# Performance work log

Measured on AMD Instinct MI355X. Metric: run time of the kernel, lower is better.

## Reference

```python
import jax, jax.numpy as jnp
import numpy as np

B, S, D, H, TM = 4, 512, 512, 8, 20
DH = D // H
LAMBDA_REG = 1e-3


def setup_inputs() -> dict:
    key = jax.random.key(0)
    ks = jax.random.split(key, 12)

    def lin(k, o, i):
        return (jax.random.normal(k, (o, i), jnp.float32) / np.float32(np.sqrt(i)))

    return {
        "x": jax.random.normal(ks[0], (B, S, D), jnp.float32),
        "Wq": lin(ks[1], D, D), "Wk": lin(ks[2], D, D), "Wv": lin(ks[3], D, D),
        "Wo": lin(ks[4], D, D), "bo": jnp.zeros((D,), jnp.float32),
        "gw1": lin(ks[5], 64, D), "gb1": jnp.zeros((64,), jnp.float32),
        "gw2": lin(ks[6], 32, 64), "gb2": jnp.zeros((32,), jnp.float32),
        "gw3": lin(ks[7], 1, 32), "gb3": jnp.zeros((1,), jnp.float32),
        "cw1": lin(ks[8], 32, D), "cb1": jnp.zeros((32,), jnp.float32),
        "cw2": lin(ks[9], 1, 32), "cb2": jnp.zeros((1,), jnp.float32),
        "alpha": jnp.float32(np.exp(-1.0 / 5.0)),   # tau_syn = 5
        "beta": jnp.float32(np.exp(-1.0 / 20.0)),   # tau_mem = 20
    }


def reference(x, Wq, Wk, Wv, Wo, bo, gw1, gb1, gw2, gb2, gw3, gb3,
              cw1, cb1, cw2, cb2, alpha, beta):
    scale = jnp.float32(DH ** -0.5)

    # adaptive window sizes T_i in [1, TM]
    g = jax.nn.sigmoid(jax.nn.relu(jax.nn.relu(x @ gw1.T + gb1) @ gw2.T + gb2) @ gw3.T + gb3)
    c = jax.nn.sigmoid(jax.nn.relu(x @ cw1.T + cb1) @ cw2.T + cb2)
    combined = (0.7 * g + 0.3 * c)[..., 0]                       # [B,S]
    T_i = jnp.clip(jnp.ceil(combined * TM), 1, TM).astype(jnp.int32)
    mask = (jnp.arange(TM)[None, None, :] < T_i[:, :, None]).astype(x.dtype)  # [B,S,TM]

    def lif_spikes(inp):  # inp [B,S,D] -> spikes [B,S,TM,D] (zeroed past T_i)
        def step(carry, _):
            v, i = carry
            i = alpha * i + inp
            v = beta * v + i
            s = jnp.where(v >= 1.0, 1.0, 0.0).astype(inp.dtype)
            v = v * (1.0 - s)  # v_reset = 0
            return (v, i), s
        z = jnp.zeros_like(inp)
        _, sp = jax.lax.scan(step, (z, z), None, length=TM)      # [TM,B,S,D]
        return jnp.moveaxis(sp, 0, 2) * mask[..., None]

    q_sp = lif_spikes(x @ Wq.T).reshape(B, S, TM, H, DH)
    k_sp = lif_spikes(x @ Wk.T).reshape(B, S, TM, H, DH)
    v_sp = lif_spikes(x @ Wv.T).reshape(B, S, TM, H, DH)

    scores = jnp.einsum('bithd,bjthd->bhij', q_sp, k_sp) * scale
    attn = jax.nn.softmax(scores, axis=-1)                       # dropout is eval-mode identity
    v_mean = v_sp.mean(axis=2).transpose(0, 2, 1, 3)             # [B,H,S,DH]
    out = jnp.einsum('bhij,bhjd->bhid', attn, v_mean)
    out = out.transpose(0, 2, 1, 3).reshape(B, S, D) @ Wo.T + bo
    reg = jnp.float32(LAMBDA_REG) * T_i.astype(x.dtype).mean()
    return out, attn, reg, T_i
```

## Files before the change

### kernel.cpp

```cpp
#include <hip/hip_runtime.h>
#include <cstdint>


typedef __attribute__((ext_vector_type(8))) _Float16 f16x8;
typedef __attribute__((ext_vector_type(4))) float f32x4;

__device__ __forceinline__ float sep_mad(float a, float b, float c) {
    float t = a * b;
    asm volatile("" : "+v"(t));
    return t + c;
}

union HU4 { _Float16 h[4]; ushort4 u; };
union HU8 { _Float16 h[8]; uint4 u; };

__device__ __forceinline__ void split4(float4 v, HU4& hi, HU4& lo) {
    hi.h[0] = (_Float16)v.x; lo.h[0] = (_Float16)(v.x - (float)hi.h[0]);
    hi.h[1] = (_Float16)v.y; lo.h[1] = (_Float16)(v.y - (float)hi.h[1]);
    hi.h[2] = (_Float16)v.z; lo.h[2] = (_Float16)(v.z - (float)hi.h[2]);
    hi.h[3] = (_Float16)v.w; lo.h[3] = (_Float16)(v.w - (float)hi.h[3]);
}

__global__ __launch_bounds__(256) void k_convert(
    const float* __restrict__ x,
    const float* __restrict__ Wq, const float* __restrict__ Wk,
    const float* __restrict__ Wv, const float* __restrict__ Wo,
    const float* __restrict__ gw1, const float* __restrict__ cw1,
    _Float16* __restrict__ xh, _Float16* __restrict__ xl,
    _Float16* __restrict__ WGh, _Float16* __restrict__ WGl,
    _Float16* __restrict__ Woh)
{
    const int t = blockIdx.x * 256 + threadIdx.x;
    HU4 hi, lo;
    if (t < 262144) {
        float4 v = ((const float4*)x)[t];
        split4(v, hi, lo);
        ((ushort4*)xh)[t] = hi.u;
        ((ushort4*)xl)[t] = lo.u;
        return;
    }
    const int t2 = t - 262144;
    if (t2 < 196608) {
        const int sel = t2 >> 16, o = t2 & 65535;
        const float* src = (sel == 0) ? Wq : ((sel == 1) ? Wk : Wv);
        float4 v = ((const float4*)src)[o];
        split4(v, hi, lo);
        ((ushort4*)WGh)[t2] = hi.u;
        ((ushort4*)WGl)[t2] = lo.u;
        return;
    }
    const int t3 = t2 - 196608;
    if (t3 < 12288) {
        const int row = t3 >> 7, c4 = t3 & 127;
        const float* src = (row < 64) ? (gw1 + row * 512) : (cw1 + (row - 64) * 512);
        float4 v = ((const float4*)src)[c4];
        split4(v, hi, lo);
        ((ushort4*)WGh)[196608 + t3] = hi.u;
        ((ushort4*)WGl)[196608 + t3] = lo.u;
        return;
    }
    const int t4 = t3 - 12288;
    if (t4 < 4096) {
        ushort4 z; z.x = z.y = z.z = z.w = 0;
        ((ushort4*)WGh)[208896 + t4] = z;
        ((ushort4*)WGl)[208896 + t4] = z;
        return;
    }
    const int t5 = t4 - 4096;
    float4 v = ((const float4*)Wo)[t5];
    split4(v, hi, lo);
    ((ushort4*)Woh)[t5] = hi.u;
}

__global__ __launch_bounds__(256) void k_gemm3(
    const _Float16* __restrict__ Ah, const _Float16* __restrict__ Al,
    const _Float16* __restrict__ Bh, const _Float16* __restrict__ Bl,
    float* __restrict__ Y)
{
    __shared__ _Float16 AsH[4][64][8];
    __shared__ _Float16 BsH[4][64][8];
    __shared__ _Float16 AsL[4][64][8];
    __shared__ _Float16 BsL[4][64][8];

    const int bn = blockIdx.x * 64, bm = blockIdx.y * 64;
    const int tid = threadIdx.x, w = tid >> 6, l = tid & 63;
    const int mB = (w & 1) * 32, nB = (w >> 1) * 32;
    const int sr = tid >> 2, sk = tid & 3;
    const int fr = l & 15, fk = l >> 4;

    f32x4 acc[2][2] = {};

    uint4 pAh = *(const uint4*)(Ah + (bm + sr) * 512 + sk * 8);
    uint4 pBh = *(const uint4*)(Bh + (bn + sr) * 512 + sk * 8);
    uint4 pAl = *(const uint4*)(Al + (bm + sr) * 512 + sk * 8);
    uint4 pBl = *(const uint4*)(Bl + (bn + sr) * 512 + sk * 8);

    for (int k0 = 0; k0 < 512; k0 += 32) {
        __syncthreads();
        *(uint4*)&AsH[sk][sr][0] = pAh;
        *(uint4*)&BsH[sk][sr][0] = pBh;
        *(uint4*)&AsL[sk][sr][0] = pAl;
        *(uint4*)&BsL[sk][sr][0] = pBl;
        __syncthreads();
        const int kn = (k0 + 32) & 511;
        pAh = *(const uint4*)(Ah + (bm + sr) * 512 + kn + sk * 8);
        pBh = *(const uint4*)(Bh + (bn + sr) * 512 + kn + sk * 8);
        pAl = *(const uint4*)(Al + (bm + sr) * 512 + kn + sk * 8);
        pBl = *(const uint4*)(Bl + (bn + sr) * 512 + kn + sk * 8);

        f16x8 ah[2], al[2];
#pragma unroll
        for (int mt = 0; mt < 2; mt++) {
            ah[mt] = *(const f16x8*)&AsH[fk][mB + mt * 16 + fr][0];
            al[mt] = *(const f16x8*)&AsL[fk][mB + mt * 16 + fr][0];
        }
#pragma unroll
        for (int nt = 0; nt < 2; nt++) {
            f16x8 bh = *(const f16x8*)&BsH[fk][nB + nt * 16 + fr][0];
            f16x8 bl = *(const f16x8*)&BsL[fk][nB + nt * 16 + fr][0];
#pragma unroll
            for (int mt = 0; mt < 2; mt++) {
                acc[mt][nt] = __builtin_amdgcn_mfma_f32_16x16x32_f16(ah[mt], bh, acc[mt][nt], 0, 0, 0);
                acc[mt][nt] = __builtin_amdgcn_mfma_f32_16x16x32_f16(ah[mt], bl, acc[mt][nt], 0, 0, 0);
                acc[mt][nt] = __builtin_amdgcn_mfma_f32_16x16x32_f16(al[mt], bh, acc[mt][nt], 0, 0, 0);
            }
        }
    }

#pragma unroll
    for (int mt = 0; mt < 2; mt++) {
#pragma unroll
        for (int nt = 0; nt < 2; nt++) {
            const int j = bn + nB + nt * 16 + fr;
#pragma unroll
            for (int rr = 0; rr < 4; rr++) {
                const int i = bm + mB + mt * 16 + fk * 4 + rr;
                Y[i * 1664 + j] = acc[mt][nt][rr];
            }
        }
    }
}

__global__ __launch_bounds__(256) void k_gates2(
    const float* __restrict__ h1raw,
    const float* __restrict__ gb1, const float* __restrict__ cb1,
    const float* __restrict__ gw2, const float* __restrict__ gb2,
    const float* __restrict__ gw3, const float* __restrict__ gb3,
    const float* __restrict__ cw2, const float* __restrict__ cb2,
    int* __restrict__ Ti, float* __restrict__ ti_out)
{
    __shared__ float h1s[32][100];
    __shared__ float w2s[32][65];
    __shared__ float h2s[32][36];
    const int tok0 = blockIdx.x * 32;
    const int tid = threadIdx.x;

    for (int i = tid; i < 2048; i += 256) w2s[i >> 6][i & 63] = gw2[i];
    for (int i = tid; i < 3072; i += 256) {
        const int r = i / 96, c = i % 96;
        const float v = h1raw[(long)(tok0 + r) * 1664 + c] + (c < 64 ? gb1[c] : cb1[c - 64]);
        h1s[r][c] = fmaxf(v, 0.f);
    }
    __syncthreads();

#pragma unroll
    for (int it = 0; it < 4; it++) {
        const int tok = (tid >> 5) + it * 8, o2 = tid & 31;
        float a = gb2[o2];
        for (int k = 0; k < 64; k++) a = fmaf(w2s[o2][k], h1s[tok][k], a);
        h2s[tok][o2] = fmaxf(a, 0.f);
    }
    __syncthreads();

    if (tid < 32) {
        const int tok = tid;
        float gg = gb3[0], cc = cb2[0];
        for (int k = 0; k < 32; k++) {
            gg = fmaf(gw3[k], h2s[tok][k], gg);
            cc = fmaf(cw2[k], h1s[tok][64 + k], cc);
        }
        float g = 1.f / (1.f + expf(-gg));
        float c = 1.f / (1.f + expf(-cc));
        float p1 = 0.7f * g, p2 = 0.3f * c;
        asm volatile("" : "+v"(p1), "+v"(p2));
        float comb = p1 + p2;
        float tf = ceilf(comb * 20.0f);
        tf = fminf(fmaxf(tf, 1.f), 20.f);
        Ti[tok0 + tok] = (int)tf;
        ti_out[tok0 + tok] = tf;
    }
}

template<int NCAT, bool BIAS>
__global__ __launch_bounds__(256) void k_gemm(
    const _Float16* __restrict__ A, const _Float16* __restrict__ B,
    const float* __restrict__ bias, float* __restrict__ Y)
{
    __shared__ _Float16 As[4][64][8];
    __shared__ _Float16 Bs[4][64][8];

    const int bn = blockIdx.x * 64, bm = blockIdx.y * 64;
    const int tid = threadIdx.x, w = tid >> 6, l = tid & 63;
    const int mB = (w & 1) * 32, nB = (w >> 1) * 32;
    const int sr = tid >> 2, sk = tid & 3;
    const int fr = l & 15, fk = l >> 4;

    f32x4 acc[2][2] = {};

    uint4 pA = *(const uint4*)(A + (bm + sr) * 512 + sk * 8);
    uint4 pB = *(const uint4*)(B + (bn + sr) * 512 + sk * 8);

    for (int k0 = 0; k0 < 512; k0 += 32) {
        __syncthreads();
        *(uint4*)&As[sk][sr][0] = pA;
        *(uint4*)&Bs[sk][sr][0] = pB;
        __syncthreads();
        const int kn = (k0 + 32) & 511;
        pA = *(const uint4*)(A + (bm + sr) * 512 + kn + sk * 8);
        pB = *(const uint4*)(B + (bn + sr) * 512 + kn + sk * 8);

        f16x8 ah[2];
#pragma unroll
        for (int mt = 0; mt < 2; mt++)
            ah[mt] = *(const f16x8*)&As[fk][mB + mt * 16 + fr][0];
#pragma unroll
        for (int nt = 0; nt < 2; nt++) {
            f16x8 bh = *(const f16x8*)&Bs[fk][nB + nt * 16 + fr][0];
#pragma unroll
            for (int mt = 0; mt < 2; mt++)
                acc[mt][nt] = __builtin_amdgcn_mfma_f32_16x16x32_f16(ah[mt], bh, acc[mt][nt], 0, 0, 0);
        }
    }

#pragma unroll
    for (int mt = 0; mt < 2; mt++) {
#pragma unroll
        for (int nt = 0; nt < 2; nt++) {
            const int j = bn + nB + nt * 16 + fr;
            float badd = BIAS ? bias[j] : 0.f;
#pragma unroll
            for (int rr = 0; rr < 4; rr++) {
                const int i = bm + mB + mt * 16 + fk * 4 + rr;
                Y[i * NCAT + j] = acc[mt][nt][rr] + badd;
            }
        }
    }
}

__global__ __launch_bounds__(256) void k_lif(
    const float* __restrict__ qkv,
    const int* __restrict__ Ti,
    const float* __restrict__ pAlpha, const float* __restrict__ pBeta,
    unsigned long long* __restrict__ qbits,
    unsigned long long* __restrict__ kbits,
    _Float16* __restrict__ vmT)
{
    __shared__ _Float16 cnts[64][18];
    const int wid = threadIdx.x >> 6, lane = threadIdx.x & 63;
    const int bh = blockIdx.y, s0 = blockIdx.x * 16;
    const int b = bh >> 3, h = bh & 7;
    const float alpha = pAlpha[0], beta = pBeta[0];

    const float* qrow0 = qkv + (long)(b * 512 + s0 + wid) * 1664 + h * 64 + lane;
    float cq = qrow0[0], ck = qrow0[512], cv = qrow0[1024];

    for (int r = 0; r < 4; r++) {
        const int tl = r * 4 + wid;
        const int s = s0 + tl;
        float nq = 0.f, nk = 0.f, nv = 0.f;
        if (r < 3) {
            const float* qr = qkv + (long)(b * 512 + s + 4) * 1664 + h * 64 + lane;
            nq = qr[0]; nk = qr[512]; nv = qr[1024];
        }
        const int T = Ti[b * 512 + s];
        float iq = 0.f, vq = 0.f, ik = 0.f, vk = 0.f, iv = 0.f, vv = 0.f;
        int cnt = 0;
        const int base = (bh * 20) * 512 + s;
#pragma unroll
        for (int t = 0; t < 20; t++) {
            iq = sep_mad(alpha, iq, cq); vq = sep_mad(beta, vq, iq);
            bool sq = vq >= 1.0f; vq = sq ? 0.f : vq;
            ik = sep_mad(alpha, ik, ck); vk = sep_mad(beta, vk, ik);
            bool sk = vk >= 1.0f; vk = sk ? 0.f : vk;
            iv = sep_mad(alpha, iv, cv); vv = sep_mad(beta, vv, iv);
            bool sv = vv >= 1.0f; vv = sv ? 0.f : vv;
            bool act = t < T;
            unsigned long long mq = __ballot(sq && act);
            unsigned long long mk = __ballot(sk && act);
            if (lane == 0) {
                qbits[base + t * 512] = mq;
                kbits[base + t * 512] = mk;
            }
            cnt += (sv && act) ? 1 : 0;
        }
        cnts[lane][tl] = (_Float16)((float)cnt / 20.0f);
        cq = nq; ck = nk; cv = nv;
    }
    __syncthreads();
    const int d = threadIdx.x >> 2, q = threadIdx.x & 3;
    HU4 o;
#pragma unroll
    for (int i = 0; i < 4; i++) o.h[i] = cnts[d][q * 4 + i];
    *(ushort4*)(vmT + (bh * 64 + d) * 512 + s0 + q * 4) = o.u;
}

__global__ __launch_bounds__(256) void k_scores(
    const unsigned long long* __restrict__ qbits,
    const unsigned long long* __restrict__ kbits,
    float* __restrict__ attn,
    const int* __restrict__ Ti, float* __restrict__ regp)
{
    const int bh = blockIdx.x >> 5;
    const int i0 = (blockIdx.x & 31) * 16;
    const int base = bh * 20 * 512;
    __shared__ unsigned long long qs[20][16];
    __shared__ float sc[16][512];
    const int tid = threadIdx.x;
    for (int idx = tid; idx < 320; idx += 256) {
        int t = idx >> 4, r = idx & 15;
        qs[t][r] = qbits[base + t * 512 + i0 + r];
    }
    int Tmax = 0;
    const int tb = (bh >> 3) * 512 + i0;
#pragma unroll
    for (int r = 0; r < 16; r++) Tmax = max(Tmax, Ti[tb + r]);
    __syncthreads();

    {
        const unsigned long long* kbp = kbits + base + tid;
        int acc0[16] = {}, acc1[16] = {};
        for (int tc = 0; tc < 4; tc++) {
            if (tc * 5 >= Tmax) break;
            unsigned long long kv0[5], kv1[5];
#pragma unroll
            for (int t = 0; t < 5; t++) {
                kv0[t] = kbp[(tc * 5 + t) * 512];
                kv1[t] = kbp[(tc * 5 + t) * 512 + 256];
            }
#pragma unroll
            for (int r = 0; r < 16; r++) {
#pragma unroll
                for (int t = 0; t < 5; t++) {
                    unsigned long long qv = qs[tc * 5 + t][r];
                    acc0[r] += __popcll(qv & kv0[t]);
                    acc1[r] += __popcll(qv & kv1[t]);
                }
            }
        }
#pragma unroll
        for (int r = 0; r < 16; r++) {
            sc[r][tid] = (float)acc0[r] * 0.125f;
            sc[r][tid + 256] = (float)acc1[r] * 0.125f;
        }
    }
    __syncthreads();

    const int wid = tid >> 6, lane = tid & 63;
#pragma unroll
    for (int rr = 0; rr < 4; rr++) {
        const int r = wid * 4 + rr;
        float vals[8];
        float m = -1e30f;
#pragma unroll
        for (int k = 0; k < 8; k++) { vals[k] = sc[r][lane + 64 * k]; m = fmaxf(m, vals[k]); }
#pragma unroll
        for (int off = 32; off; off >>= 1) m = fmaxf(m, __shfl_xor(m, off));
        float sum = 0.f;
#pragma unroll
        for (int k = 0; k < 8; k++) { vals[k] = expf(vals[k] - m); sum += vals[k]; }
#pragma unroll
        for (int off = 32; off; off >>= 1) sum += __shfl_xor(sum, off);
        float* arow = attn + ((long)bh * 512 + (i0 + r)) * 512;
#pragma unroll
        for (int k = 0; k < 8; k++) arow[lane + 64 * k] = vals[k] / sum;
    }

    if (blockIdx.x == 0 && tid < 64) {
        int s = 0;
        for (int k = tid; k < 2048; k += 64) s += Ti[k];
#pragma unroll
        for (int off = 32; off; off >>= 1) s += __shfl_xor(s, off);
        if (tid == 0) regp[0] = 1e-3f * ((float)s / 2048.0f);
    }
}

__global__ __launch_bounds__(256) void k_av(
    const float* __restrict__ attn,
    const _Float16* __restrict__ vmT,
    _Float16* __restrict__ hout)
{
    __shared__ _Float16 Aa[4][64][8];
    __shared__ _Float16 Bb[4][64][8];
    const int i0 = blockIdx.x * 64;
    const int bh = blockIdx.y;
    const int b = bh >> 3, h = bh & 7;
    const int tid = threadIdx.x, w = tid >> 6, l = tid & 63;
    const int mB = (w & 1) * 32, nB = (w >> 1) * 32;
    const int sr = tid >> 2, sk = tid & 3;
    const int fr = l & 15, fk = l >> 4;
    const float* abase = attn + ((long)bh * 512 + i0) * 512;
    const _Float16* bbase = vmT + bh * 64 * 512;

    f32x4 acc[2][2] = {};

    float4 pa0 = *(const float4*)(abase + sr * 512 + sk * 8);
    float4 pa1 = *(const float4*)(abase + sr * 512 + sk * 8 + 4);
    uint4 pb = *(const uint4*)(bbase + sr * 512 + sk * 8);

    for (int k0 = 0; k0 < 512; k0 += 32) {
        __syncthreads();
        {
            HU8 z;
            z.h[0] = (_Float16)pa0.x; z.h[1] = (_Float16)pa0.y;
            z.h[2] = (_Float16)pa0.z; z.h[3] = (_Float16)pa0.w;
            z.h[4] = (_Float16)pa1.x; z.h[5] = (_Float16)pa1.y;
            z.h[6] = (_Float16)pa1.z; z.h[7] = (_Float16)pa1.w;
            *(uint4*)&Aa[sk][sr][0] = z.u;
            *(uint4*)&Bb[sk][sr][0] = pb;
        }
        __syncthreads();
        const int kn = (k0 + 32) & 511;
        pa0 = *(const float4*)(abase + sr * 512 + kn + sk * 8);
        pa1 = *(const float4*)(abase + sr * 512 + kn + sk * 8 + 4);
        pb = *(const uint4*)(bbase + sr * 512 + kn + sk * 8);

        f16x8 ah[2];
#pragma unroll
        for (int mt = 0; mt < 2; mt++)
            ah[mt] = *(const f16x8*)&Aa[fk][mB + mt * 16 + fr][0];
#pragma unroll
        for (int nt = 0; nt < 2; nt++) {
            f16x8 bv = *(const f16x8*)&Bb[fk][nB + nt * 16 + fr][0];
#pragma unroll
            for (int mt = 0; mt < 2; mt++)
                acc[mt][nt] = __builtin_amdgcn_mfma_f32_16x16x32_f16(ah[mt], bv, acc[mt][nt], 0, 0, 0);
        }
    }

#pragma unroll
    for (int mt = 0; mt < 2; mt++) {
#pragma unroll
        for (int nt = 0; nt < 2; nt++) {
            const int d = nB + nt * 16 + fr;
#pragma unroll
            for (int rr = 0; rr < 4; rr++) {
                const int i = i0 + mB + mt * 16 + fk * 4 + rr;
                hout[(b * 512 + i) * 512 + h * 64 + d] = (_Float16)acc[mt][nt][rr];
            }
        }
    }
}

extern "C" void kernel_launch(void* const* d_in, const int* in_sizes, int n_in,
                              void* d_out, int out_size, void* d_ws, size_t ws_size,
                              hipStream_t stream)
{
    const float* x    = (const float*)d_in[0];
    const float* Wq   = (const float*)d_in[1];
    const float* Wk   = (const float*)d_in[2];
    const float* Wv   = (const float*)d_in[3];
    const float* Wo   = (const float*)d_in[4];
    const float* bo   = (const float*)d_in[5];
    const float* gw1  = (const float*)d_in[6];
    const float* gb1  = (const float*)d_in[7];
    const float* gw2  = (const float*)d_in[8];
    const float* gb2  = (const float*)d_in[9];
    const float* gw3  = (const float*)d_in[10];
    const float* gb3  = (const float*)d_in[11];
    const float* cw1  = (const float*)d_in[12];
    const float* cb1  = (const float*)d_in[13];
    const float* cw2  = (const float*)d_in[14];
    const float* cb2  = (const float*)d_in[15];
    const float* alpha = (const float*)d_in[16];
    const float* beta  = (const float*)d_in[17];

    float* out   = (float*)d_out;
    float* attn  = out + 1048576;
    float* regp  = out + 1048576 + 8388608;
    float* tiout = regp + 1;

    char* ws = (char*)d_ws;
    float*    qkvh1  = (float*)ws;
    unsigned long long* qb = (unsigned long long*)(ws + 13631488);
    unsigned long long* kb = (unsigned long long*)(ws + 16252928);
    _Float16* vmT    = (_Float16*)(ws + 18874368);
    _Float16* hout_h = (_Float16*)(ws + 20971520);
    int*      Ti     = (int*)(ws + 23068672);
    _Float16* xh     = (_Float16*)(ws + 23076864);
    _Float16* xl     = (_Float16*)(ws + 25174016);
    _Float16* WGh    = (_Float16*)(ws + 27271168);
    _Float16* WGl    = (_Float16*)(ws + 28975104);
    _Float16* Woh    = (_Float16*)(ws + 30679040);

    k_convert<<<2112, 256, 0, stream>>>(x, Wq, Wk, Wv, Wo, gw1, cw1,
                                        xh, xl, WGh, WGl, Woh);
    k_gemm3<<<dim3(26, 32), 256, 0, stream>>>(xh, xl, WGh, WGl, qkvh1);
    k_gates2<<<64, 256, 0, stream>>>(qkvh1 + 1536, gb1, cb1, gw2, gb2, gw3, gb3,
                                     cw2, cb2, Ti, tiout);
    k_lif<<<dim3(32, 32), 256, 0, stream>>>(qkvh1, Ti, alpha, beta, qb, kb, vmT);
    k_scores<<<1024, 256, 0, stream>>>(qb, kb, attn, Ti, regp);
    k_av<<<dim3(8, 32), 256, 0, stream>>>(attn, vmT, hout_h);
    k_gemm<512, true><<<dim3(8, 32), 256, 0, stream>>>(hout_h, Woh, bo, out);
}
```

Baseline: 114.2 us.

## Fuse fp16 split conversion into GEMMs and gate MLP into LIF kernel

Removes the separate conversion kernel by having the QKV GEMM load fp32 x and weights and split them into hi/lo fp16 in-register before staging to shared memory. The Wo GEMM now converts Wo to fp16 on the fly. The gate MLP kernel is merged into the LIF kernel, so each block recomputes T_i for its 16 tokens, once per head, and reads it from shared memory. The score kernel's k-bit loads become 128-bit vector loads with an interleaved column mapping. This cuts two launches and the intermediate fp16 buffers. In exchange, conversion work is repeated across tiles and the gate MLP is computed eight times.

```diff
diff --git a/kernel.cpp b/kernel.cpp
--- a/kernel.cpp
+++ b/kernel.cpp
@@ -21,60 +21,11 @@
     hi.h[3] = (_Float16)v.w; lo.h[3] = (_Float16)(v.w - (float)hi.h[3]);
 }
 
-__global__ __launch_bounds__(256) void k_convert(
-    const float* __restrict__ x,
+__global__ __launch_bounds__(256) void k_gemm3(
+    const float* __restrict__ X,
     const float* __restrict__ Wq, const float* __restrict__ Wk,
-    const float* __restrict__ Wv, const float* __restrict__ Wo,
-    const float* __restrict__ gw1, const float* __restrict__ cw1,
-    _Float16* __restrict__ xh, _Float16* __restrict__ xl,
-    _Float16* __restrict__ WGh, _Float16* __restrict__ WGl,
-    _Float16* __restrict__ Woh)
-{
-    const int t = blockIdx.x * 256 + threadIdx.x;
-    HU4 hi, lo;
-    if (t < 262144) {
-        float4 v = ((const float4*)x)[t];
-        split4(v, hi, lo);
-        ((ushort4*)xh)[t] = hi.u;
-        ((ushort4*)xl)[t] = lo.u;
-        return;
-    }
-    const int t2 = t - 262144;
-    if (t2 < 196608) {
-        const int sel = t2 >> 16, o = t2 & 65535;
-        const float* src = (sel == 0) ? Wq : ((sel == 1) ? Wk : Wv);
-        float4 v = ((const float4*)src)[o];
-        split4(v, hi, lo);
-        ((ushort4*)WGh)[t2] = hi.u;
-        ((ushort4*)WGl)[t2] = lo.u;
-        return;
-    }
-    const int t3 = t2 - 196608;
-    if (t3 < 12288) {
-        const int row = t3 >> 7, c4 = t3 & 127;
-        const float* src = (row < 64) ? (gw1 + row * 512) : (cw1 + (row - 64) * 512);
-        float4 v = ((const float4*)src)[c4];
-        split4(v, hi, lo);
-        ((ushort4*)WGh)[196608 + t3] = hi.u;
-        ((ushort4*)WGl)[196608 + t3] = lo.u;
-        return;
-    }
-    const int t4 = t3 - 12288;
-    if (t4 < 4096) {
-        ushort4 z; z.x = z.y = z.z = z.w = 0;
-        ((ushort4*)WGh)[208896 + t4] = z;
-        ((ushort4*)WGl)[208896 + t4] = z;
-        return;
-    }
-    const int t5 = t4 - 4096;
-    float4 v = ((const float4*)Wo)[t5];
-    split4(v, hi, lo);
-    ((ushort4*)Woh)[t5] = hi.u;
-}
-
-__global__ __launch_bounds__(256) void k_gemm3(
-    const _Float16* __restrict__ Ah, const _Float16* __restrict__ Al,
-    const _Float16* __restrict__ Bh, const _Float16* __restrict__ Bl,
+    const float* __restrict__ Wv, const float* __restrict__ gw1,
+    const float* __restrict__ cw1,
     float* __restrict__ Y)
 {
     __shared__ _Float16 AsH[4][64][8];
@@ -88,25 +39,44 @@
     const int sr = tid >> 2, sk = tid & 3;
     const int fr = l & 15, fk = l >> 4;
 
+    const float* asrc = X + (bm + sr) * 512;
+    const int brow = bn + sr;
+    const float* bsrc;
+    bool bvalid = true;
+    if      (brow < 512)  bsrc = Wq  + brow * 512;
+    else if (brow < 1024) bsrc = Wk  + (brow - 512) * 512;
+    else if (brow < 1536) bsrc = Wv  + (brow - 1024) * 512;
+    else if (brow < 1600) bsrc = gw1 + (brow - 1536) * 512;
+    else if (brow < 1632) bsrc = cw1 + (brow - 1600) * 512;
+    else { bsrc = Wq; bvalid = false; }
+
     f32x4 acc[2][2] = {};
-
-    uint4 pAh = *(const uint4*)(Ah + (bm + sr) * 512 + sk * 8);
-    uint4 pBh = *(const uint4*)(Bh + (bn + sr) * 512 + sk * 8);
-    uint4 pAl = *(const uint4*)(Al + (bm + sr) * 512 + sk * 8);
-    uint4 pBl = *(const uint4*)(Bl + (bn + sr) * 512 + sk * 8);
+    const float4 z4{0.f, 0.f, 0.f, 0.f};
+
+    float4 pa0 = *(const float4*)(asrc + sk * 8);
+    float4 pa1 = *(const float4*)(asrc + sk * 8 + 4);
+    float4 pb0 = bvalid ? *(const float4*)(bsrc + sk * 8)     : z4;
+    float4 pb1 = bvalid ? *(const float4*)(bsrc + sk * 8 + 4) : z4;
 
     for (int k0 = 0; k0 < 512; k0 += 32) {
         __syncthreads();
-        *(uint4*)&AsH[sk][sr][0] = pAh;
-        *(uint4*)&BsH[sk][sr][0] = pBh;
-        *(uint4*)&AsL[sk][sr][0] = pAl;
-        *(uint4*)&BsL[sk][sr][0] = pBl;
+        {
+            HU4 h0, l0, h1, l1;
+            split4(pa0, h0, l0); split4(pa1, h1, l1);
+            *(ushort4*)&AsH[sk][sr][0] = h0.u; *(ushort4*)&AsH[sk][sr][4] = h1.u;
+            *(ushort4*)&AsL[sk][sr][0] = l0.u; *(ushort4*)&AsL[sk][sr][4] = l1.u;
+            split4(pb0, h0, l0); split4(pb1, h1, l1);
+            *(ushort4*)&BsH[sk][sr][0] = h0.u; *(ushort4*)&BsH[sk][sr][4] = h1.u;
+            *(ushort4*)&BsL[sk][sr][0] = l0.u; *(ushort4*)&BsL[sk][sr][4] = l1.u;
+        }
         __syncthreads();
         const int kn = (k0 + 32) & 511;
-        pAh = *(const uint4*)(Ah + (bm + sr) * 512 + kn + sk * 8);
-        pBh = *(const uint4*)(Bh + (bn + sr) * 512 + kn + sk * 8);
-        pAl = *(const uint4*)(Al + (bm + sr) * 512 + kn + sk * 8);
-        pBl = *(const uint4*)(Bl + (bn + sr) * 512 + kn + sk * 8);
+        pa0 = *(const float4*)(asrc + kn + sk * 8);
+        pa1 = *(const float4*)(asrc + kn + sk * 8 + 4);
+        if (bvalid) {
+            pb0 = *(const float4*)(bsrc + kn + sk * 8);
+            pb1 = *(const float4*)(bsrc + kn + sk * 8 + 4);
+        }
 
         f16x8 ah[2], al[2];
 #pragma unroll
@@ -141,38 +111,46 @@
     }
 }
 
-__global__ __launch_bounds__(256) void k_gates2(
-    const float* __restrict__ h1raw,
+__global__ __launch_bounds__(256) void k_lif(
+    const float* __restrict__ qkvh1,
     const float* __restrict__ gb1, const float* __restrict__ cb1,
     const float* __restrict__ gw2, const float* __restrict__ gb2,
     const float* __restrict__ gw3, const float* __restrict__ gb3,
     const float* __restrict__ cw2, const float* __restrict__ cb2,
+    const float* __restrict__ pAlpha, const float* __restrict__ pBeta,
+    unsigned long long* __restrict__ qbits,
+    unsigned long long* __restrict__ kbits,
+    _Float16* __restrict__ vmT,
     int* __restrict__ Ti, float* __restrict__ ti_out)
 {
-    __shared__ float h1s[32][100];
-    __shared__ float w2s[32][65];
-    __shared__ float h2s[32][36];
-    const int tok0 = blockIdx.x * 32;
+    __shared__ _Float16 cnts[64][18];
+    __shared__ float h1s[16][100];
+    __shared__ float h2s[16][36];
+    __shared__ int tis[16];
     const int tid = threadIdx.x;
-
-    for (int i = tid; i < 2048; i += 256) w2s[i >> 6][i & 63] = gw2[i];
-    for (int i = tid; i < 3072; i += 256) {
+    const int wid = tid >> 6, lane = tid & 63;
+    const int bh = blockIdx.y, s0 = blockIdx.x * 16;
+    const int b = bh >> 3, h = bh & 7;
+    const float alpha = pAlpha[0], beta = pBeta[0];
+
+    for (int i = tid; i < 1536; i += 256) {
         const int r = i / 96, c = i % 96;
-        const float v = h1raw[(long)(tok0 + r) * 1664 + c] + (c < 64 ? gb1[c] : cb1[c - 64]);
+        const float v = qkvh1[(long)(b * 512 + s0 + r) * 1664 + 1536 + c]
+                        + (c < 64 ? gb1[c] : cb1[c - 64]);
         h1s[r][c] = fmaxf(v, 0.f);
     }
     __syncthreads();
-
-#pragma unroll
-    for (int it = 0; it < 4; it++) {
-        const int tok = (tid >> 5) + it * 8, o2 = tid & 31;
+#pragma unroll
+    for (int ii = 0; ii < 2; ii++) {
+        const int idx = tid + ii * 256;
+        const int tok = idx >> 5, o2 = idx & 31;
+        const float* w2 = gw2 + o2 * 64;
         float a = gb2[o2];
-        for (int k = 0; k < 64; k++) a = fmaf(w2s[o2][k], h1s[tok][k], a);
+        for (int k = 0; k < 64; k++) a = fmaf(w2[k], h1s[tok][k], a);
         h2s[tok][o2] = fmaxf(a, 0.f);
     }
     __syncthreads();
-
-    if (tid < 32) {
+    if (tid < 16) {
         const int tok = tid;
         float gg = gb3[0], cc = cb2[0];
         for (int k = 0; k < 32; k++) {
@@ -186,82 +164,13 @@
         float comb = p1 + p2;
         float tf = ceilf(comb * 20.0f);
         tf = fminf(fmaxf(tf, 1.f), 20.f);
-        Ti[tok0 + tok] = (int)tf;
-        ti_out[tok0 + tok] = tf;
-    }
-}
-
-template<int NCAT, bool BIAS>
-__global__ __launch_bounds__(256) void k_gemm(
-    const _Float16* __restrict__ A, const _Float16* __restrict__ B,
-    const float* __restrict__ bias, float* __restrict__ Y)
-{
-    __shared__ _Float16 As[4][64][8];
-    __shared__ _Float16 Bs[4][64][8];
-
-    const int bn = blockIdx.x * 64, bm = blockIdx.y * 64;
-    const int tid = threadIdx.x, w = tid >> 6, l = tid & 63;
-    const int mB = (w & 1) * 32, nB = (w >> 1) * 32;
-    const int sr = tid >> 2, sk = tid & 3;
-    const int fr = l & 15, fk = l >> 4;
-
-    f32x4 acc[2][2] = {};
-
-    uint4 pA = *(const uint4*)(A + (bm + sr) * 512 + sk * 8);
-    uint4 pB = *(const uint4*)(B + (bn + sr) * 512 + sk * 8);
-
-    for (int k0 = 0; k0 < 512; k0 += 32) {
-        __syncthreads();
-        *(uint4*)&As[sk][sr][0] = pA;
-        *(uint4*)&Bs[sk][sr][0] = pB;
-        __syncthreads();
-        const int kn = (k0 + 32) & 511;
-        pA = *(const uint4*)(A + (bm + sr) * 512 + kn + sk * 8);
-        pB = *(const uint4*)(B + (bn + sr) * 512 + kn + sk * 8);
-
-        f16x8 ah[2];
-#pragma unroll
-        for (int mt = 0; mt < 2; mt++)
-            ah[mt] = *(const f16x8*)&As[fk][mB + mt * 16 + fr][0];
-#pragma unroll
-        for (int nt = 0; nt < 2; nt++) {
-            f16x8 bh = *(const f16x8*)&Bs[fk][nB + nt * 16 + fr][0];
-#pragma unroll
-            for (int mt = 0; mt < 2; mt++)
-                acc[mt][nt] = __builtin_amdgcn_mfma_f32_16x16x32_f16(ah[mt], bh, acc[mt][nt], 0, 0, 0);
-        }
-    }
-
-#pragma unroll
-    for (int mt = 0; mt < 2; mt++) {
-#pragma unroll
-        for (int nt = 0; nt < 2; nt++) {
-            const int j = bn + nB + nt * 16 + fr;
-            float badd = BIAS ? bias[j] : 0.f;
-#pragma unroll
-            for (int rr = 0; rr < 4; rr++) {
-                const int i = bm + mB + mt * 16 + fk * 4 + rr;
-                Y[i * NCAT + j] = acc[mt][nt][rr] + badd;
-            }
-        }
-    }
-}
-
-__global__ __launch_bounds__(256) void k_lif(
-    const float* __restrict__ qkv,
-    const int* __restrict__ Ti,
-    const float* __restrict__ pAlpha, const float* __restrict__ pBeta,
-    unsigned long long* __restrict__ qbits,
-    unsigned long long* __restrict__ kbits,
-    _Float16* __restrict__ vmT)
-{
-    __shared__ _Float16 cnts[64][18];
-    const int wid = threadIdx.x >> 6, lane = threadIdx.x & 63;
-    const int bh = blockIdx.y, s0 = blockIdx.x * 16;
-    const int b = bh >> 3, h = bh & 7;
-    const float alpha = pAlpha[0], beta = pBeta[0];
-
-    const float* qrow0 = qkv + (long)(b * 512 + s0 + wid) * 1664 + h * 64 + lane;
+        tis[tok] = (int)tf;
+        Ti[b * 512 + s0 + tok] = (int)tf;
+        ti_out[b * 512 + s0 + tok] = tf;
+    }
+    __syncthreads();
+
+    const float* qrow0 = qkvh1 + (long)(b * 512 + s0 + wid) * 1664 + h * 64 + lane;
     float cq = qrow0[0], ck = qrow0[512], cv = qrow0[1024];
 
     for (int r = 0; r < 4; r++) {
@@ -269,10 +178,10 @@
         const int s = s0 + tl;
         float nq = 0.f, nk = 0.f, nv = 0.f;
         if (r < 3) {
-            const float* qr = qkv + (long)(b * 512 + s + 4) * 1664 + h * 64 + lane;
+            const float* qr = qkvh1 + (long)(b * 512 + s + 4) * 1664 + h * 64 + lane;
             nq = qr[0]; nk = qr[512]; nv = qr[1024];
         }
-        const int T = Ti[b * 512 + s];
+        const int T = tis[tl];
         float iq = 0.f, vq = 0.f, ik = 0.f, vk = 0.f, iv = 0.f, vv = 0.f;
         int cnt = 0;
         const int base = (bh * 20) * 512 + s;
@@ -297,7 +206,7 @@
         cq = nq; ck = nk; cv = nv;
     }
     __syncthreads();
-    const int d = threadIdx.x >> 2, q = threadIdx.x & 3;
+    const int d = tid >> 2, q = tid & 3;
     HU4 o;
 #pragma unroll
     for (int i = 0; i < 4; i++) o.h[i] = cnts[d][q * 4 + i];
@@ -327,15 +236,15 @@
     __syncthreads();
 
     {
-        const unsigned long long* kbp = kbits + base + tid;
+        const unsigned long long* kbp = kbits + base + 2 * tid;
         int acc0[16] = {}, acc1[16] = {};
         for (int tc = 0; tc < 4; tc++) {
             if (tc * 5 >= Tmax) break;
             unsigned long long kv0[5], kv1[5];
 #pragma unroll
             for (int t = 0; t < 5; t++) {
-                kv0[t] = kbp[(tc * 5 + t) * 512];
-                kv1[t] = kbp[(tc * 5 + t) * 512 + 256];
+                ulonglong2 kk = *(const ulonglong2*)(kbp + (tc * 5 + t) * 512);
+                kv0[t] = kk.x; kv1[t] = kk.y;
             }
 #pragma unroll
             for (int r = 0; r < 16; r++) {
@@ -349,8 +258,8 @@
         }
 #pragma unroll
         for (int r = 0; r < 16; r++) {
-            sc[r][tid] = (float)acc0[r] * 0.125f;
-            sc[r][tid + 256] = (float)acc1[r] * 0.125f;
+            sc[r][2 * tid]     = (float)acc0[r] * 0.125f;
+            sc[r][2 * tid + 1] = (float)acc1[r] * 0.125f;
         }
     }
     __syncthreads();
@@ -446,6 +355,71 @@
             for (int rr = 0; rr < 4; rr++) {
                 const int i = i0 + mB + mt * 16 + fk * 4 + rr;
                 hout[(b * 512 + i) * 512 + h * 64 + d] = (_Float16)acc[mt][nt][rr];
+            }
+        }
+    }
+}
+
+__global__ __launch_bounds__(256) void k_gemmWo(
+    const _Float16* __restrict__ A, const float* __restrict__ Wo,
+    const float* __restrict__ bias, float* __restrict__ Y)
+{
+    __shared__ _Float16 As[4][64][8];
+    __shared__ _Float16 Bs[4][64][8];
+
+    const int bn = blockIdx.x * 64, bm = blockIdx.y * 64;
+    const int tid = threadIdx.x, w = tid >> 6, l = tid & 63;
+    const int mB = (w & 1) * 32, nB = (w >> 1) * 32;
+    const int sr = tid >> 2, sk = tid & 3;
+    const int fr = l & 15, fk = l >> 4;
+
+    f32x4 acc[2][2] = {};
+
+    const float* bsrc = Wo + (bn + sr) * 512;
+    uint4 pA = *(const uint4*)(A + (bm + sr) * 512 + sk * 8);
+    float4 pb0 = *(const float4*)(bsrc + sk * 8);
+    float4 pb1 = *(const float4*)(bsrc + sk * 8 + 4);
+
+    for (int k0 = 0; k0 < 512; k0 += 32) {
+        __syncthreads();
+        {
+            HU8 z;
+            z.h[0] = (_Float16)pb0.x; z.h[1] = (_Float16)pb0.y;
+            z.h[2] = (_Float16)pb0.z; z.h[3] = (_Float16)pb0.w;
+            z.h[4] = (_Float16)pb1.x; z.h[5] = (_Float16)pb1.y;
+            z.h[6] = (_Float16)pb1.z; z.h[7] = (_Float16)pb1.w;
+            *(uint4*)&As[sk][sr][0] = pA;
+            *(uint4*)&Bs[sk][sr][0] = z.u;
+        }
+        __syncthreads();
+        const int kn = (k0 + 32) & 511;
+        pA = *(const uint4*)(A + (bm + sr) * 512 + kn + sk * 8);
+        pb0 = *(const float4*)(bsrc + kn + sk * 8);
+        pb1 = *(const float4*)(bsrc + kn + sk * 8 + 4);
+
+        f16x8 ah[2];
+#pragma unroll
+        for (int mt = 0; mt < 2; mt++)
+            ah[mt] = *(const f16x8*)&As[fk][mB + mt * 16 + fr][0];
+#pragma unroll
+        for (int nt = 0; nt < 2; nt++) {
+            f16x8 bh = *(const f16x8*)&Bs[fk][nB + nt * 16 + fr][0];
+#pragma unroll
+            for (int mt = 0; mt < 2; mt++)
+                acc[mt][nt] = __builtin_amdgcn_mfma_f32_16x16x32_f16(ah[mt], bh, acc[mt][nt], 0, 0, 0);
+        }
+    }
+
+#pragma unroll
+    for (int mt = 0; mt < 2; mt++) {
+#pragma unroll
+        for (int nt = 0; nt < 2; nt++) {
+            const int j = bn + nB + nt * 16 + fr;
+            const float badd = bias[j];
+#pragma unroll
+            for (int rr = 0; rr < 4; rr++) {
+                const int i = bm + mB + mt * 16 + fk * 4 + rr;
+                Y[i * 512 + j] = acc[mt][nt][rr] + badd;
             }
         }
     }
@@ -486,19 +460,11 @@
     _Float16* vmT    = (_Float16*)(ws + 18874368);
     _Float16* hout_h = (_Float16*)(ws + 20971520);
     int*      Ti     = (int*)(ws + 23068672);
-    _Float16* xh     = (_Float16*)(ws + 23076864);
-    _Float16* xl     = (_Float16*)(ws + 25174016);
-    _Float16* WGh    = (_Float16*)(ws + 27271168);
-    _Float16* WGl    = (_Float16*)(ws + 28975104);
-    _Float16* Woh    = (_Float16*)(ws + 30679040);
-
-    k_convert<<<2112, 256, 0, stream>>>(x, Wq, Wk, Wv, Wo, gw1, cw1,
-                                        xh, xl, WGh, WGl, Woh);
-    k_gemm3<<<dim3(26, 32), 256, 0, stream>>>(xh, xl, WGh, WGl, qkvh1);
-    k_gates2<<<64, 256, 0, stream>>>(qkvh1 + 1536, gb1, cb1, gw2, gb2, gw3, gb3,
-                                     cw2, cb2, Ti, tiout);
-    k_lif<<<dim3(32, 32), 256, 0, stream>>>(qkvh1, Ti, alpha, beta, qb, kb, vmT);
+
+    k_gemm3<<<dim3(26, 32), 256, 0, stream>>>(x, Wq, Wk, Wv, gw1, cw1, qkvh1);
+    k_lif<<<dim3(32, 32), 256, 0, stream>>>(qkvh1, gb1, cb1, gw2, gb2, gw3, gb3,
+                                            cw2, cb2, alpha, beta, qb, kb, vmT, Ti, tiout);
     k_scores<<<1024, 256, 0, stream>>>(qb, kb, attn, Ti, regp);
     k_av<<<dim3(8, 32), 256, 0, stream>>>(attn, vmT, hout_h);
-    k_gemm<512, true><<<dim3(8, 32), 256, 0, stream>>>(hout_h, Woh, bo, out);
-}
+    k_gemmWo<<<dim3(8, 32), 256, 0, stream>>>(hout_h, Wo, bo, out);
+}
```

Result: slower. 130.5 us (+14.2%).
